# Performance work log

Measured on AMD Instinct MI355X. Metric: run time of the kernel, lower is better.

## Reference

```python
import math
import jax, jax.numpy as jnp
import numpy as np

jax.config.update("jax_enable_x64", True)

P_PRIME = 1000003            # prime modulus; p-1 = 2*3*166667
N_FACTORS = (2, 3, 166667)   # prime factors of p-1 (for primitive-root search)
B, NPATCH, L, K, DIM = 4, 784, 9, 16, 28  # batch, patches/sample, patch len, kernels, map dim


def _modpow(base, exp, p, nbits=21):
    """Vectorized modular exponentiation (square-and-multiply), int64, exponents < 2^nbits."""
    shape = jnp.broadcast_shapes(jnp.shape(base), jnp.shape(exp))
    b0 = jnp.broadcast_to(jnp.asarray(base, jnp.int64) % p, shape)
    e = jnp.broadcast_to(jnp.asarray(exp, jnp.int64), shape)
    def body(i, c):
        res, b = c
        res = jnp.where(((e >> i) & 1) == 1, (res * b) % p, res)
        return (res, (b * b) % p)
    res, _ = jax.lax.fori_loop(0, nbits, body, (jnp.ones(shape, jnp.int64), b0))
    return res


def _decrypt_ips(ct0, cts, y, sk_y, g, p):
    """IPFE decrypt + BSGS discrete log. ct0:[B,P] cts:[B,P,L] y:[K,L] sk_y:[K] -> signed ip [K,B,P]."""
    n = p - 1
    powed = _modpow(cts[None], jnp.mod(y, n)[:, None, None, :], p)   # [K,B,P,L]
    num = powed[..., 0]
    for i in range(1, L):                                            # fixed small L=9
        num = (num * powed[..., i]) % p
    denom = _modpow(ct0[None], jnp.mod(sk_y, n)[:, None, None], p)   # [K,B,P]
    val = (num * _modpow(denom, p - 2, p)) % p                       # = g^{<x,y>} mod p (Fermat inverse)
    # baby-step giant-step over group order n
    m = math.isqrt(n - 1) + 1
    n_giant = -(-n // m)
    baby = _modpow(jnp.int64(g), jnp.arange(m, dtype=jnp.int64), p)  # g^j, j in [0,m)
    order = jnp.argsort(baby)
    sb = baby[order]
    ginv_m = _modpow(jnp.int64(g), jnp.int64((n - m) % n), p)        # g^{-m}
    pt = _modpow(ginv_m, jnp.arange(n_giant, dtype=jnp.int64), p)    # g^{-m*i}
    gamma = (val.reshape(-1)[:, None] * pt[None, :]) % p             # [T, n_giant] giant steps
    pos = jnp.clip(jnp.searchsorted(sb, gamma), 0, m - 1)
    hit = sb[pos] == gamma
    cand = jnp.arange(n_giant, dtype=jnp.int64)[None, :] * m + order[pos]
    ip = jnp.min(jnp.where(hit, cand, n), axis=1)                    # unique match: ip = i*m + j
    ip = jnp.where(ip > n // 2, ip - n, ip)                          # signed representative
    return ip.reshape(K, ct0.shape[0], ct0.shape[1])


def _bn(x, g_, b_, m_, v_):
    s = g_ * jax.lax.rsqrt(v_ + 1e-5)
    return (x - m_[None, :, None, None]) * s[None, :, None, None] + b_[None, :, None, None]


def _conv(x, w, b):
    o = jax.lax.conv_general_dilated(x, w, (1, 1), ((1, 1), (1, 1)),
                                     dimension_numbers=("NCHW", "OIHW", "NCHW"))
    return o + b[None, :, None, None]


def _pool(x):
    return jax.lax.reduce_window(x, jnp.array(-jnp.inf, x.dtype), jax.lax.max,
                                 (1, 1, 2, 2), (1, 1, 2, 2), "VALID")


def _forward(ct0, cts, y, sk_y, bias1, bn1_g, bn1_b, bn1_m, bn1_v,
             conv2_w, conv2_b, bn2_g, bn2_b, bn2_m, bn2_v,
             conv3_w, conv3_b, bn3_g, bn3_b, bn3_m, bn3_v,
             fc1_w, fc1_b, fc2_w, fc2_b, g, p):
    ip = _decrypt_ips(ct0, cts, y, sk_y, g, p)                       # [K,B,P] int64
    maps = ip.astype(jnp.float32) / 10000.0 + bias1[:, None, None]   # dequantize + conv1 bias
    feat = jnp.transpose(maps, (1, 0, 2)).reshape(-1, K, DIM, DIM)   # [B,16,28,28]
    feat = _pool(jax.nn.relu(_bn(feat, bn1_g, bn1_b, bn1_m, bn1_v)))
    feat = _pool(jax.nn.relu(_bn(_conv(feat, conv2_w, conv2_b), bn2_g, bn2_b, bn2_m, bn2_v)))
    feat = _pool(jax.nn.relu(_bn(_conv(feat, conv3_w, conv3_b), bn3_g, bn3_b, bn3_m, bn3_v)))
    flat = feat.reshape(feat.shape[0], -1)                           # [B,576]
    h = jax.nn.relu(flat @ fc1_w.T + fc1_b)                          # dropout = identity (eval mode)
    return h @ fc2_w.T + fc2_b                                       # [B,10]


def setup_inputs():
    rng = np.random.default_rng(0)
    p, n = P_PRIME, P_PRIME - 1
    assert all(p % d for d in range(2, math.isqrt(p) + 1))           # p prime
    g = next(gg for gg in range(2, 200)
             if all(pow(gg, n // q, p) != 1 for q in N_FACTORS))      # primitive root mod p
    s = rng.integers(1, n, size=L)                                    # master secret
    pk = [pow(g, int(si), p) for si in s]
    y = rng.integers(-50, 51, size=(K, L)).astype(np.int64)          # round(w*10000)
    x = rng.integers(0, 21, size=(B, NPATCH, L))                     # quantized patch values
    r = rng.integers(1, n, size=(B, NPATCH))
    gx = [pow(g, t, p) for t in range(21)]
    ct0 = np.zeros((B, NPATCH), dtype=np.int64)
    cts = np.zeros((B, NPATCH, L), dtype=np.int64)
    for b in range(B):
        for j in range(NPATCH):
            rr = int(r[b, j])
            ct0[b, j] = pow(g, rr, p)
            for i in range(L):
                cts[b, j, i] = pow(pk[i], rr, p) * gx[x[b, j, i]] % p
    sk_y = np.array([sum(int(s[i]) * int(y[k, i]) for i in range(L)) % n
                     for k in range(K)], dtype=np.int64)
    f32 = lambda a: jnp.asarray(a, jnp.float32)
    def rn(*sh):
        return f32(rng.standard_normal(sh) * 0.1)
    def bnp(c):
        return (f32(1.0 + 0.1 * rng.standard_normal(c)), rn(c), rn(c), f32(rng.random(c) + 0.5))
    bn1_g, bn1_b, bn1_m, bn1_v = bnp(16)
    bn2_g, bn2_b, bn2_m, bn2_v = bnp(32)
    bn3_g, bn3_b, bn3_m, bn3_v = bnp(64)
    return dict(ct0=jnp.asarray(ct0), cts=jnp.asarray(cts),
                y=jnp.asarray(y), sk_y=jnp.asarray(sk_y), bias1=rn(K),
                bn1_g=bn1_g, bn1_b=bn1_b, bn1_m=bn1_m, bn1_v=bn1_v,
                conv2_w=rn(32, 16, 3, 3), conv2_b=rn(32),
                bn2_g=bn2_g, bn2_b=bn2_b, bn2_m=bn2_m, bn2_v=bn2_v,
                conv3_w=rn(64, 32, 3, 3), conv3_b=rn(64),
                bn3_g=bn3_g, bn3_b=bn3_b, bn3_m=bn3_m, bn3_v=bn3_v,
                fc1_w=rn(128, 576), fc1_b=rn(128),
                fc2_w=rn(10, 128), fc2_b=rn(10), g=g, p=p)


def reference(ct0, cts, y, sk_y, bias1, bn1_g, bn1_b, bn1_m, bn1_v,
              conv2_w, conv2_b, bn2_g, bn2_b, bn2_m, bn2_v,
              conv3_w, conv3_b, bn3_g, bn3_b, bn3_m, bn3_v,
              fc1_w, fc1_b, fc2_w, fc2_b, g, p):
    return _forward(ct0, cts, y, sk_y, bias1, bn1_g, bn1_b, bn1_m, bn1_v,
                    conv2_w, conv2_b, bn2_g, bn2_b, bn2_m, bn2_v,
                    conv3_w, conv3_b, bn3_g, bn3_b, bn3_m, bn3_v,
                    fc1_w, fc1_b, fc2_w, fc2_b, g, p)
```

## Files before the change

### kernel.cpp

```cpp
#include <hip/hip_runtime.h>
#include <stdint.h>

#define PRIME 1000003u
#define NORD  1000002u
#define KCH   16
#define BATCH 4
#define NPATCH 784
#define LLEN  9
#define IPMAX 9000
#define TBLN  (2*IPMAX+1)

__device__ __forceinline__ uint32_t mmul(uint32_t a, uint32_t b) {
    uint64_t t = (uint64_t)a * (uint64_t)b;
    uint32_t q = (uint32_t)((t * 2199016ull) >> 41);
    uint32_t r = (uint32_t)t - q * PRIME;
    return (r >= PRIME) ? r - PRIME : r;
}

__device__ uint32_t mpow(uint32_t base, uint32_t exp) {
    uint32_t r = 1u, b = base;
    while (exp) {
        if (exp & 1u) r = mmul(r, b);
        b = mmul(b, b);
        exp >>= 1;
    }
    return r;
}

__global__ void build_table(const int* __restrict__ g_in, int* __restrict__ table) {
    int e = blockIdx.x * blockDim.x + threadIdx.x;
    if (e >= TBLN) return;
    int es = e - IPMAX;
    uint32_t exp = (es >= 0) ? (uint32_t)es : (uint32_t)(es + (int)NORD);
    uint32_t v = mpow((uint32_t)g_in[0], exp);
    table[v] = es;
}

__global__ void decrypt(const int* __restrict__ ct0, const int* __restrict__ cts,
                        const int* __restrict__ y, const int* __restrict__ sk_y,
                        const float* __restrict__ bias1,
                        const int* __restrict__ table, float* __restrict__ feat) {
    int t = blockIdx.x * blockDim.x + threadIdx.x;
    if (t >= KCH * BATCH * NPATCH) return;
    int k = t / (BATCH * NPATCH);
    int r = t % (BATCH * NPATCH);
    int b = r / NPATCH;
    int j = r % NPATCH;

    const int* crow = cts + ((b * NPATCH) + j) * LLEN;
    const int* yrow = y + k * LLEN;

    uint32_t num_p = 1u, num_n = 1u;
#pragma unroll
    for (int i = 0; i < LLEN; i++) {
        int yi = yrow[i];
        uint32_t c = (uint32_t)crow[i];
        if (yi > 0)       num_p = mmul(num_p, mpow(c, (uint32_t)yi));
        else if (yi < 0)  num_n = mmul(num_n, mpow(c, (uint32_t)(-yi)));
    }
    uint32_t den = mpow((uint32_t)ct0[b * NPATCH + j], (uint32_t)sk_y[k]);
    den = mmul(den, num_n);
    uint32_t val = mmul(num_p, mpow(den, PRIME - 2u));

    int ip = table[val];
    feat[((b * KCH) + k) * NPATCH + j] = (float)ip * 1e-4f + bias1[k];
}

__global__ void __launch_bounds__(256) stage1(
    const float* __restrict__ feat,
    const float* __restrict__ bn1_g, const float* __restrict__ bn1_b,
    const float* __restrict__ bn1_m, const float* __restrict__ bn1_v,
    float* __restrict__ s1g) {
    int idx = blockIdx.x * 256 + threadIdx.x;
    if (idx >= BATCH * 16 * 196) return;
    int b = idx / (16 * 196);
    int r = idx % (16 * 196);
    int c = r / 196;
    int pos = r % 196;
    int oh = pos / 14, ow = pos % 14;
    float sc = bn1_g[c] * rsqrtf(bn1_v[c] + 1e-5f);
    float sh = bn1_b[c] - bn1_m[c] * sc;
    const float* fp = feat + ((b * KCH) + c) * NPATCH;
    float x00 = fp[(2 * oh) * 28 + 2 * ow];
    float x01 = fp[(2 * oh) * 28 + 2 * ow + 1];
    float x10 = fp[(2 * oh + 1) * 28 + 2 * ow];
    float x11 = fp[(2 * oh + 1) * 28 + 2 * ow + 1];
    float m = fmaxf(fmaxf(x00, x01), fmaxf(x10, x11));
    s1g[idx] = fmaxf(m * sc + sh, 0.0f);
}

__global__ void __launch_bounds__(256) stage1_safe(
    const float* __restrict__ feat,
    const float* __restrict__ bn1_g, const float* __restrict__ bn1_b,
    const float* __restrict__ bn1_m, const float* __restrict__ bn1_v,
    float* __restrict__ s1g) {
    int idx = blockIdx.x * 256 + threadIdx.x;
    if (idx >= BATCH * 16 * 196) return;
    int b = idx / (16 * 196);
    int r = idx % (16 * 196);
    int c = r / 196;
    int pos = r % 196;
    int oh = pos / 14, ow = pos % 14;
    float sc = bn1_g[c] * rsqrtf(bn1_v[c] + 1e-5f);
    float sh = bn1_b[c] - bn1_m[c] * sc;
    const float* fp = feat + ((b * KCH) + c) * NPATCH;
    float m = -1e30f;
#pragma unroll
    for (int dy = 0; dy < 2; dy++)
#pragma unroll
        for (int dx = 0; dx < 2; dx++) {
            float x = fp[(2 * oh + dy) * 28 + (2 * ow + dx)];
            m = fmaxf(m, fmaxf(x * sc + sh, 0.0f));
        }
    s1g[idx] = m;
}

__global__ void __launch_bounds__(256) conv2_k(
    const float* __restrict__ s1g,
    const float* __restrict__ conv2_w, const float* __restrict__ conv2_b,
    const float* __restrict__ bn2_g, const float* __restrict__ bn2_b,
    const float* __restrict__ bn2_m, const float* __restrict__ bn2_v,
    float* __restrict__ s2g) {
    const int b  = blockIdx.x >> 5;
    const int oc = blockIdx.x & 31;
    const int tid = threadIdx.x;

    __shared__ float s1p[16][16][16];
    __shared__ float w[16 * 9];
    __shared__ float co[196];

    for (int i = tid; i < 16 * 16 * 16; i += 256)
        ((float*)s1p)[i] = 0.0f;
    if (tid < 144) w[tid] = conv2_w[oc * 144 + tid];
    __syncthreads();
    for (int i = tid; i < 16 * 196; i += 256) {
        int ic = i / 196, pos = i % 196;
        int yy = pos / 14, xx = pos % 14;
        s1p[ic][yy + 1][xx + 1] = s1g[((b * 16 + ic) * 196) + pos];
    }
    __syncthreads();

    if (tid < 196) {
        int oh = tid / 14, ow = tid % 14;
        float a0 = 0.0f, a1 = 0.0f, a2 = 0.0f;
#pragma unroll
        for (int ic = 0; ic < 16; ic++) {
            const float* wp = &w[ic * 9];
            const float* sp = &s1p[ic][oh][ow];
            a0 = fmaf(sp[0],  wp[0], fmaf(sp[1],  wp[1], fmaf(sp[2],  wp[2], a0)));
            a1 = fmaf(sp[16], wp[3], fmaf(sp[17], wp[4], fmaf(sp[18], wp[5], a1)));
            a2 = fmaf(sp[32], wp[6], fmaf(sp[33], wp[7], fmaf(sp[34], wp[8], a2)));
        }
        float sc = bn2_g[oc] * rsqrtf(bn2_v[oc] + 1e-5f);
        float sh = bn2_b[oc] - bn2_m[oc] * sc;
        float acc = (a0 + a1 + a2 + conv2_b[oc]) * sc + sh;
        co[tid] = fmaxf(acc, 0.0f);
    }
    __syncthreads();

    if (tid < 49) {
        int oh = tid / 7, ow = tid % 7;
        const float* c0 = &co[(2 * oh) * 14 + 2 * ow];
        float mx = fmaxf(fmaxf(c0[0], c0[1]), fmaxf(c0[14], c0[15]));
        s2g[((b * 32 + oc) * 49) + tid] = mx;
    }
}

__global__ void __launch_bounds__(64) conv3_k(
    const float* __restrict__ s2g,
    const float* __restrict__ conv3_w, const float* __restrict__ conv3_b,
    const float* __restrict__ bn3_g, const float* __restrict__ bn3_b,
    const float* __restrict__ bn3_m, const float* __restrict__ bn3_v,
    float* __restrict__ s3g) {
    const int b  = blockIdx.x >> 6;
    const int oc = blockIdx.x & 63;
    const int tid = threadIdx.x;

    __shared__ float s2p[32][9][9];
    __shared__ float w[32 * 9];
    __shared__ float co[49];

    for (int i = tid; i < 32 * 81; i += 64)
        ((float*)s2p)[i] = 0.0f;
    for (int i = tid; i < 288; i += 64) w[i] = conv3_w[oc * 288 + i];
    __syncthreads();
    for (int i = tid; i < 32 * 49; i += 64) {
        int ic = i / 49, pos = i % 49;
        int yy = pos / 7, xx = pos % 7;
        s2p[ic][yy + 1][xx + 1] = s2g[((b * 32 + ic) * 49) + pos];
    }
    __syncthreads();

    if (tid < 49) {
        int oh = tid / 7, ow = tid % 7;
        float a0 = 0.0f, a1 = 0.0f, a2 = 0.0f;
#pragma unroll
        for (int ic = 0; ic < 32; ic++) {
            const float* wp = &w[ic * 9];
            const float* sp = &s2p[ic][oh][ow];
            a0 = fmaf(sp[0],  wp[0], fmaf(sp[1],  wp[1], fmaf(sp[2],  wp[2], a0)));
            a1 = fmaf(sp[9],  wp[3], fmaf(sp[10], wp[4], fmaf(sp[11], wp[5], a1)));
            a2 = fmaf(sp[18], wp[6], fmaf(sp[19], wp[7], fmaf(sp[20], wp[8], a2)));
        }
        float sc = bn3_g[oc] * rsqrtf(bn3_v[oc] + 1e-5f);
        float sh = bn3_b[oc] - bn3_m[oc] * sc;
        float acc = (a0 + a1 + a2 + conv3_b[oc]) * sc + sh;
        co[tid] = fmaxf(acc, 0.0f);
    }
    __syncthreads();

    if (tid < 9) {
        int oh = tid / 3, ow = tid % 3;
        const float* c0 = &co[(2 * oh) * 7 + 2 * ow];
        float mx = fmaxf(fmaxf(c0[0], c0[1]), fmaxf(c0[7], c0[8]));
        s3g[b * 576 + oc * 9 + tid] = mx;
    }
}

__global__ void __launch_bounds__(128) fc_k(
    const float* __restrict__ s3g,
    const float* __restrict__ fc1_w, const float* __restrict__ fc1_b,
    const float* __restrict__ fc2_w, const float* __restrict__ fc2_b,
    float* __restrict__ out) {
    const int b = blockIdx.x;
    const int tid = threadIdx.x;
    __shared__ float s3[576];
    __shared__ float h[128];

    for (int i = tid; i < 576; i += 128) s3[i] = s3g[b * 576 + i];
    __syncthreads();

    {
        float a0 = 0.0f, a1 = 0.0f, a2 = 0.0f, a3 = 0.0f;
        const float* w = fc1_w + tid * 576;
        for (int i = 0; i < 576; i += 4) {
            a0 = fmaf(s3[i],     w[i],     a0);
            a1 = fmaf(s3[i + 1], w[i + 1], a1);
            a2 = fmaf(s3[i + 2], w[i + 2], a2);
            a3 = fmaf(s3[i + 3], w[i + 3], a3);
        }
        h[tid] = fmaxf(a0 + a1 + a2 + a3 + fc1_b[tid], 0.0f);
    }
    __syncthreads();

    if (tid < 10) {
        float a0 = 0.0f, a1 = 0.0f;
        const float* w = fc2_w + tid * 128;
        for (int i = 0; i < 128; i += 2) {
            a0 = fmaf(h[i],     w[i],     a0);
            a1 = fmaf(h[i + 1], w[i + 1], a1);
        }
        out[b * 10 + tid] = a0 + a1 + fc2_b[tid];
    }
}

extern "C" void kernel_launch(void* const* d_in, const int* in_sizes, int n_in,
                              void* d_out, int out_size, void* d_ws, size_t ws_size,
                              hipStream_t stream) {
    const int*   ct0    = (const int*)d_in[0];
    const int*   cts    = (const int*)d_in[1];
    const int*   y      = (const int*)d_in[2];
    const int*   sk_y   = (const int*)d_in[3];
    const float* bias1  = (const float*)d_in[4];
    const float* bn1_g  = (const float*)d_in[5];
    const float* bn1_b  = (const float*)d_in[6];
    const float* bn1_m  = (const float*)d_in[7];
    const float* bn1_v  = (const float*)d_in[8];
    const float* conv2_w = (const float*)d_in[9];
    const float* conv2_b = (const float*)d_in[10];
    const float* bn2_g  = (const float*)d_in[11];
    const float* bn2_b  = (const float*)d_in[12];
    const float* bn2_m  = (const float*)d_in[13];
    const float* bn2_v  = (const float*)d_in[14];
    const float* conv3_w = (const float*)d_in[15];
    const float* conv3_b = (const float*)d_in[16];
    const float* bn3_g  = (const float*)d_in[17];
    const float* bn3_b  = (const float*)d_in[18];
    const float* bn3_m  = (const float*)d_in[19];
    const float* bn3_v  = (const float*)d_in[20];
    const float* fc1_w  = (const float*)d_in[21];
    const float* fc1_b  = (const float*)d_in[22];
    const float* fc2_w  = (const float*)d_in[23];
    const float* fc2_b  = (const float*)d_in[24];
    const int*   g_in   = (const int*)d_in[25];
    float* out = (float*)d_out;

    char* ws = (char*)d_ws;
    int*   table = (int*)ws;
    float* feat  = (float*)(ws + 4000256);
    float* s1g   = (float*)(ws + 4200960);
    float* s2g   = (float*)(ws + 4251136);
    float* s3g   = (float*)(ws + 4276224);

    build_table<<<(TBLN + 255) / 256, 256, 0, stream>>>(g_in, table);

    int ndec = KCH * BATCH * NPATCH;
    decrypt<<<(ndec + 255) / 256, 256, 0, stream>>>(ct0, cts, y, sk_y, bias1, table, feat);

    stage1_safe<<<(BATCH * 16 * 196 + 255) / 256, 256, 0, stream>>>(
        feat, bn1_g, bn1_b, bn1_m, bn1_v, s1g);

    conv2_k<<<BATCH * 32, 256, 0, stream>>>(
        s1g, conv2_w, conv2_b, bn2_g, bn2_b, bn2_m, bn2_v, s2g);

    conv3_k<<<BATCH * 64, 64, 0, stream>>>(
        s2g, conv3_w, conv3_b, bn3_g, bn3_b, bn3_m, bn3_v, s3g);

    fc_k<<<BATCH, 128, 0, stream>>>(s3g, fc1_w, fc1_b, fc2_w, fc2_b, out);
}
```

Before: 152.4 us.

## Fuse BN1/ReLU into decrypt, pool into conv2, conv3 with FC layers

Applies the bias, BN1 and ReLU directly in the decrypt kernel and moves the 2x2 max-pool into conv2's shared-memory load, which removes the separate stage1 kernel. Conv3 and both FC layers now run in a single per-batch kernel with 256 threads, cutting launches from six to four and dropping the s1g and s3g round trips. mpow is force-inlined. The trade-off is that conv3 now runs on only 4 blocks, so each block does far more serial work and much less of the GPU is used.

```diff
diff --git a/kernel.cpp b/kernel.cpp
--- a/kernel.cpp
+++ b/kernel.cpp
@@ -17,7 +17,7 @@
     return (r >= PRIME) ? r - PRIME : r;
 }
 
-__device__ uint32_t mpow(uint32_t base, uint32_t exp) {
+__device__ __forceinline__ uint32_t mpow(uint32_t base, uint32_t exp) {
     uint32_t r = 1u, b = base;
     while (exp) {
         if (exp & 1u) r = mmul(r, b);
@@ -36,10 +36,13 @@
     table[v] = es;
 }
 
-__global__ void decrypt(const int* __restrict__ ct0, const int* __restrict__ cts,
-                        const int* __restrict__ y, const int* __restrict__ sk_y,
-                        const float* __restrict__ bias1,
-                        const int* __restrict__ table, float* __restrict__ feat) {
+__global__ void __launch_bounds__(256) decrypt(
+    const int* __restrict__ ct0, const int* __restrict__ cts,
+    const int* __restrict__ y, const int* __restrict__ sk_y,
+    const float* __restrict__ bias1,
+    const float* __restrict__ bn1_g, const float* __restrict__ bn1_b,
+    const float* __restrict__ bn1_m, const float* __restrict__ bn1_v,
+    const int* __restrict__ table, float* __restrict__ featr) {
     int t = blockIdx.x * blockDim.x + threadIdx.x;
     if (t >= KCH * BATCH * NPATCH) return;
     int k = t / (BATCH * NPATCH);
@@ -63,60 +66,15 @@
     uint32_t val = mmul(num_p, mpow(den, PRIME - 2u));
 
     int ip = table[val];
-    feat[((b * KCH) + k) * NPATCH + j] = (float)ip * 1e-4f + bias1[k];
-}
-
-__global__ void __launch_bounds__(256) stage1(
-    const float* __restrict__ feat,
-    const float* __restrict__ bn1_g, const float* __restrict__ bn1_b,
-    const float* __restrict__ bn1_m, const float* __restrict__ bn1_v,
-    float* __restrict__ s1g) {
-    int idx = blockIdx.x * 256 + threadIdx.x;
-    if (idx >= BATCH * 16 * 196) return;
-    int b = idx / (16 * 196);
-    int r = idx % (16 * 196);
-    int c = r / 196;
-    int pos = r % 196;
-    int oh = pos / 14, ow = pos % 14;
-    float sc = bn1_g[c] * rsqrtf(bn1_v[c] + 1e-5f);
-    float sh = bn1_b[c] - bn1_m[c] * sc;
-    const float* fp = feat + ((b * KCH) + c) * NPATCH;
-    float x00 = fp[(2 * oh) * 28 + 2 * ow];
-    float x01 = fp[(2 * oh) * 28 + 2 * ow + 1];
-    float x10 = fp[(2 * oh + 1) * 28 + 2 * ow];
-    float x11 = fp[(2 * oh + 1) * 28 + 2 * ow + 1];
-    float m = fmaxf(fmaxf(x00, x01), fmaxf(x10, x11));
-    s1g[idx] = fmaxf(m * sc + sh, 0.0f);
-}
-
-__global__ void __launch_bounds__(256) stage1_safe(
-    const float* __restrict__ feat,
-    const float* __restrict__ bn1_g, const float* __restrict__ bn1_b,
-    const float* __restrict__ bn1_m, const float* __restrict__ bn1_v,
-    float* __restrict__ s1g) {
-    int idx = blockIdx.x * 256 + threadIdx.x;
-    if (idx >= BATCH * 16 * 196) return;
-    int b = idx / (16 * 196);
-    int r = idx % (16 * 196);
-    int c = r / 196;
-    int pos = r % 196;
-    int oh = pos / 14, ow = pos % 14;
-    float sc = bn1_g[c] * rsqrtf(bn1_v[c] + 1e-5f);
-    float sh = bn1_b[c] - bn1_m[c] * sc;
-    const float* fp = feat + ((b * KCH) + c) * NPATCH;
-    float m = -1e30f;
-#pragma unroll
-    for (int dy = 0; dy < 2; dy++)
-#pragma unroll
-        for (int dx = 0; dx < 2; dx++) {
-            float x = fp[(2 * oh + dy) * 28 + (2 * ow + dx)];
-            m = fmaxf(m, fmaxf(x * sc + sh, 0.0f));
-        }
-    s1g[idx] = m;
+
+    float sc = bn1_g[k] * rsqrtf(bn1_v[k] + 1e-5f);
+    float sh = (bias1[k] - bn1_m[k]) * sc + bn1_b[k];
+    float v_ = fmaf((float)ip, sc * 1e-4f, sh);
+    featr[((b * KCH) + k) * NPATCH + j] = fmaxf(v_, 0.0f);
 }
 
 __global__ void __launch_bounds__(256) conv2_k(
-    const float* __restrict__ s1g,
+    const float* __restrict__ featr,
     const float* __restrict__ conv2_w, const float* __restrict__ conv2_b,
     const float* __restrict__ bn2_g, const float* __restrict__ bn2_b,
     const float* __restrict__ bn2_m, const float* __restrict__ bn2_v,
@@ -136,7 +94,9 @@
     for (int i = tid; i < 16 * 196; i += 256) {
         int ic = i / 196, pos = i % 196;
         int yy = pos / 14, xx = pos % 14;
-        s1p[ic][yy + 1][xx + 1] = s1g[((b * 16 + ic) * 196) + pos];
+        const float* fp = featr + ((b * 16 + ic) * 784) + (2 * yy) * 28 + 2 * xx;
+        float m = fmaxf(fmaxf(fp[0], fp[1]), fmaxf(fp[28], fp[29]));
+        s1p[ic][yy + 1][xx + 1] = m;
     }
     __syncthreads();
 
@@ -166,86 +126,85 @@
     }
 }
 
-__global__ void __launch_bounds__(64) conv3_k(
+__global__ void __launch_bounds__(256) conv3fc_k(
     const float* __restrict__ s2g,
     const float* __restrict__ conv3_w, const float* __restrict__ conv3_b,
     const float* __restrict__ bn3_g, const float* __restrict__ bn3_b,
     const float* __restrict__ bn3_m, const float* __restrict__ bn3_v,
-    float* __restrict__ s3g) {
-    const int b  = blockIdx.x >> 6;
-    const int oc = blockIdx.x & 63;
-    const int tid = threadIdx.x;
-
-    __shared__ float s2p[32][9][9];
-    __shared__ float w[32 * 9];
-    __shared__ float co[49];
-
-    for (int i = tid; i < 32 * 81; i += 64)
-        ((float*)s2p)[i] = 0.0f;
-    for (int i = tid; i < 288; i += 64) w[i] = conv3_w[oc * 288 + i];
-    __syncthreads();
-    for (int i = tid; i < 32 * 49; i += 64) {
-        int ic = i / 49, pos = i % 49;
-        int yy = pos / 7, xx = pos % 7;
-        s2p[ic][yy + 1][xx + 1] = s2g[((b * 32 + ic) * 49) + pos];
-    }
-    __syncthreads();
-
-    if (tid < 49) {
-        int oh = tid / 7, ow = tid % 7;
-        float a0 = 0.0f, a1 = 0.0f, a2 = 0.0f;
-#pragma unroll
-        for (int ic = 0; ic < 32; ic++) {
-            const float* wp = &w[ic * 9];
-            const float* sp = &s2p[ic][oh][ow];
-            a0 = fmaf(sp[0],  wp[0], fmaf(sp[1],  wp[1], fmaf(sp[2],  wp[2], a0)));
-            a1 = fmaf(sp[9],  wp[3], fmaf(sp[10], wp[4], fmaf(sp[11], wp[5], a1)));
-            a2 = fmaf(sp[18], wp[6], fmaf(sp[19], wp[7], fmaf(sp[20], wp[8], a2)));
-        }
-        float sc = bn3_g[oc] * rsqrtf(bn3_v[oc] + 1e-5f);
-        float sh = bn3_b[oc] - bn3_m[oc] * sc;
-        float acc = (a0 + a1 + a2 + conv3_b[oc]) * sc + sh;
-        co[tid] = fmaxf(acc, 0.0f);
-    }
-    __syncthreads();
-
-    if (tid < 9) {
-        int oh = tid / 3, ow = tid % 3;
-        const float* c0 = &co[(2 * oh) * 7 + 2 * ow];
-        float mx = fmaxf(fmaxf(c0[0], c0[1]), fmaxf(c0[7], c0[8]));
-        s3g[b * 576 + oc * 9 + tid] = mx;
-    }
-}
-
-__global__ void __launch_bounds__(128) fc_k(
-    const float* __restrict__ s3g,
     const float* __restrict__ fc1_w, const float* __restrict__ fc1_b,
     const float* __restrict__ fc2_w, const float* __restrict__ fc2_b,
     float* __restrict__ out) {
     const int b = blockIdx.x;
     const int tid = threadIdx.x;
+
+    __shared__ float s2p[32][9][9];
+    __shared__ float co[64][49];
     __shared__ float s3[576];
+    __shared__ float hp[256];
     __shared__ float h[128];
 
-    for (int i = tid; i < 576; i += 128) s3[i] = s3g[b * 576 + i];
+    for (int i = tid; i < 32 * 81; i += 256)
+        ((float*)s2p)[i] = 0.0f;
+    __syncthreads();
+    for (int i = tid; i < 32 * 49; i += 256) {
+        int ic = i / 49, pos = i % 49;
+        s2p[ic][pos / 7 + 1][pos % 7 + 1] = s2g[(b * 32 + ic) * 49 + pos];
+    }
     __syncthreads();
 
     {
+        const int oc = tid >> 2;
+        const int q  = tid & 3;
+        const float* wb = conv3_w + oc * 288;
+        float sc = bn3_g[oc] * rsqrtf(bn3_v[oc] + 1e-5f);
+        float sh = bn3_b[oc] - bn3_m[oc] * sc;
+        float cb = conv3_b[oc];
+        for (int pos = q; pos < 49; pos += 4) {
+            int oh = pos / 7, ow = pos % 7;
+            float a0 = 0.0f, a1 = 0.0f, a2 = 0.0f;
+#pragma unroll
+            for (int ic = 0; ic < 32; ic++) {
+                const float* wp = wb + ic * 9;
+                const float* sp = &s2p[ic][oh][ow];
+                a0 = fmaf(sp[0],  wp[0], fmaf(sp[1],  wp[1], fmaf(sp[2],  wp[2], a0)));
+                a1 = fmaf(sp[9],  wp[3], fmaf(sp[10], wp[4], fmaf(sp[11], wp[5], a1)));
+                a2 = fmaf(sp[18], wp[6], fmaf(sp[19], wp[7], fmaf(sp[20], wp[8], a2)));
+            }
+            float acc = (a0 + a1 + a2 + cb) * sc + sh;
+            co[oc][pos] = fmaxf(acc, 0.0f);
+        }
+    }
+    __syncthreads();
+
+    for (int i = tid; i < 576; i += 256) {
+        int oc = i / 9, pp = i % 9;
+        int oh = pp / 3, ow = pp % 3;
+        const float* c0 = &co[oc][(2 * oh) * 7 + 2 * ow];
+        s3[i] = fmaxf(fmaxf(c0[0], c0[1]), fmaxf(c0[7], c0[8]));
+    }
+    __syncthreads();
+
+    {
+        const int o = tid >> 1;
+        const int half = tid & 1;
+        const float* w = fc1_w + o * 576 + half * 288;
+        const float* x = s3 + half * 288;
         float a0 = 0.0f, a1 = 0.0f, a2 = 0.0f, a3 = 0.0f;
-        const float* w = fc1_w + tid * 576;
-        for (int i = 0; i < 576; i += 4) {
-            a0 = fmaf(s3[i],     w[i],     a0);
-            a1 = fmaf(s3[i + 1], w[i + 1], a1);
-            a2 = fmaf(s3[i + 2], w[i + 2], a2);
-            a3 = fmaf(s3[i + 3], w[i + 3], a3);
-        }
-        h[tid] = fmaxf(a0 + a1 + a2 + a3 + fc1_b[tid], 0.0f);
-    }
+        for (int i = 0; i < 288; i += 4) {
+            a0 = fmaf(x[i],     w[i],     a0);
+            a1 = fmaf(x[i + 1], w[i + 1], a1);
+            a2 = fmaf(x[i + 2], w[i + 2], a2);
+            a3 = fmaf(x[i + 3], w[i + 3], a3);
+        }
+        hp[tid] = a0 + a1 + a2 + a3;
+    }
+    __syncthreads();
+    if (tid < 128) h[tid] = fmaxf(hp[2 * tid] + hp[2 * tid + 1] + fc1_b[tid], 0.0f);
     __syncthreads();
 
     if (tid < 10) {
+        const float* w = fc2_w + tid * 128;
         float a0 = 0.0f, a1 = 0.0f;
-        const float* w = fc2_w + tid * 128;
         for (int i = 0; i < 128; i += 2) {
             a0 = fmaf(h[i],     w[i],     a0);
             a1 = fmaf(h[i + 1], w[i + 1], a1);
@@ -287,24 +246,19 @@
 
     char* ws = (char*)d_ws;
     int*   table = (int*)ws;
-    float* feat  = (float*)(ws + 4000256);
-    float* s1g   = (float*)(ws + 4200960);
-    float* s2g   = (float*)(ws + 4251136);
-    float* s3g   = (float*)(ws + 4276224);
+    float* featr = (float*)(ws + 4000256);
+    float* s2g   = (float*)(ws + 4200960);
 
     build_table<<<(TBLN + 255) / 256, 256, 0, stream>>>(g_in, table);
 
     int ndec = KCH * BATCH * NPATCH;
-    decrypt<<<(ndec + 255) / 256, 256, 0, stream>>>(ct0, cts, y, sk_y, bias1, table, feat);
-
-    stage1_safe<<<(BATCH * 16 * 196 + 255) / 256, 256, 0, stream>>>(
-        feat, bn1_g, bn1_b, bn1_m, bn1_v, s1g);
+    decrypt<<<(ndec + 255) / 256, 256, 0, stream>>>(
+        ct0, cts, y, sk_y, bias1, bn1_g, bn1_b, bn1_m, bn1_v, table, featr);
 
     conv2_k<<<BATCH * 32, 256, 0, stream>>>(
-        s1g, conv2_w, conv2_b, bn2_g, bn2_b, bn2_m, bn2_v, s2g);
-
-    conv3_k<<<BATCH * 64, 64, 0, stream>>>(
-        s2g, conv3_w, conv3_b, bn3_g, bn3_b, bn3_m, bn3_v, s3g);
-
-    fc_k<<<BATCH, 128, 0, stream>>>(s3g, fc1_w, fc1_b, fc2_w, fc2_b, out);
-}
+        featr, conv2_w, conv2_b, bn2_g, bn2_b, bn2_m, bn2_v, s2g);
+
+    conv3fc_k<<<BATCH, 256, 0, stream>>>(
+        s2g, conv3_w, conv3_b, bn3_g, bn3_b, bn3_m, bn3_v,
+        fc1_w, fc1_b, fc2_w, fc2_b, out);
+}
```

After: 195.4 us. 28.3% more time.
